# Optimization experiments

Measured on AMD Instinct MI355X. Metric: run time of the kernel, lower is better.

## Reference

```python
import jax, jax.numpy as jnp
import numpy as np

MARGIN = 0.2  # self.margin; temperature is unused in the original forward


def setup_inputs() -> dict:
    key = jax.random.key(0)
    k1, k2 = jax.random.split(key)
    B, D, NUM_CLASSES = 512, 256, 10
    features = jax.random.normal(k1, (B, D), dtype=jnp.float32)
    labels = jax.random.randint(k2, (B,), 0, NUM_CLASSES, dtype=jnp.int32)
    return {"features": features, "labels": labels}


def reference(features, labels):
    B = features.shape[0]
    sim = features @ features.T  # [B, B]

    eq = (labels[:, None] == labels[None, :])
    pos_mask = eq.astype(sim.dtype) * (1.0 - jnp.eye(B, dtype=sim.dtype))  # diag zeroed
    neg_mask = 1.0 - eq.astype(sim.dtype)

    # For anchor row i, pos j, neg k: relu(margin + sim[i,k] - sim[i,j])
    hinge = jax.nn.relu(MARGIN + sim[:, None, :] - sim[:, :, None])  # [B, Bpos, Bneg]
    loss_sum = jnp.einsum('ijk,ij,ik->', hinge, pos_mask, neg_mask)

    pos_cnt = pos_mask.sum(axis=1)  # per-row positive counts
    neg_cnt = neg_mask.sum(axis=1)
    valid = (pos_cnt > 0) & (neg_cnt > 0)
    num_valid = valid.sum().astype(sim.dtype)

    # Original bug faithfully reproduced: denominator uses the LAST row's
    # pos/neg counts (pos_sim/neg_sim leak out of the python loop).
    denom = num_valid * pos_cnt[-1] * neg_cnt[-1]
    return jnp.where(denom > 0, loss_sum / denom, jnp.zeros((), sim.dtype))
```

## Files before the change

kernel.cpp:

```cpp
#include <hip/hip_runtime.h>

#define B 512
#define D 256
#define NCLS 10
#define MARGIN 0.2f
#define THREADS 1024
#define NWAVES (THREADS / 64)
#define ROWS 2
#define NBLOCKS (B / ROWS)
#define DT 32
#define NDT (D / DT)
#define TILE_FLOATS (B * DT)

__global__ __launch_bounds__(THREADS) void fused_loss_kernel(
    const float* __restrict__ F, const int* __restrict__ labels,
    float* __restrict__ out)
{
    __shared__ float  buf[2][TILE_FLOATS];
    __shared__ float2 part[2][B];
    __shared__ float  pos_vals[ROWS][B + 4];
    __shared__ float  neg_vals[ROWS][B];
    __shared__ int    lbl[B];
    __shared__ int    cnt[ROWS][2];
    __shared__ int    hist[NCLS];
    __shared__ float  wred[NWAVES];
    __shared__ int    vred[NWAVES];

    const int t    = threadIdx.x;
    const int lane = t & 63;
    const int w    = t >> 6;
    const int i0   = blockIdx.x * ROWS;
    const int h    = t >> 9;
    const int j    = t & (B - 1);
    const int sj   = (j & 7) ^ ((j >> 3) & 7);
    const int h4   = __builtin_amdgcn_readfirstlane(h << 2);

    auto stage = [&](float* dstbase, int tile) {
#pragma unroll
        for (int k = 0; k < 4; ++k) {
            const int p  = (w << 8) + (k << 6) + lane;
            const int jj = p >> 3;
            const int e4 = (p & 7) ^ (jj & 7) ^ ((jj >> 3) & 7);
            const float* src = F + jj * D + tile * DT + (e4 << 2);
            float* dst = dstbase + (w << 10) + (k << 8);
            __builtin_amdgcn_global_load_lds(
                (const __attribute__((address_space(1))) void*)src,
                (__attribute__((address_space(3))) void*)dst, 16, 0, 0);
        }
    };

    if (t < B)        lbl[t] = labels[t];
    if (t < NCLS)     hist[t] = 0;
    if (t < ROWS * 2) ((int*)cnt)[t] = 0;
    stage(buf[0], 0);

    asm volatile("s_waitcnt lgkmcnt(0)" ::: "memory");
    __builtin_amdgcn_s_barrier();

    if (t < B) atomicAdd(&hist[lbl[t]], 1);

    float acc0 = 0.f, acc1 = 0.f;
    const float* Fa0 = F + (size_t)i0 * D;
    const float* Fa1 = Fa0 + D;
    int cur = 0;
    for (int tile = 0; tile < NDT; ++tile) {
        if (tile + 1 < NDT) {
            stage(buf[cur ^ 1], tile + 1);
            asm volatile("s_waitcnt vmcnt(4)" ::: "memory");
        } else {
            asm volatile("s_waitcnt vmcnt(0)" ::: "memory");
        }
        __builtin_amdgcn_s_barrier();
        __builtin_amdgcn_sched_barrier(0);
        const float* bufc = buf[cur];
        const int dt = tile * DT;
#pragma unroll
        for (int k = 0; k < 4; ++k) {
            const int e4 = h4 + k;
            const float4 x  = *(const float4*)&bufc[(j << 5) + ((e4 ^ sj) << 2)];
            const float4 a0 = *(const float4*)&Fa0[dt + (e4 << 2)];
            const float4 a1 = *(const float4*)&Fa1[dt + (e4 << 2)];
            acc0 = fmaf(a0.x, x.x, acc0); acc0 = fmaf(a0.y, x.y, acc0);
            acc0 = fmaf(a0.z, x.z, acc0); acc0 = fmaf(a0.w, x.w, acc0);
            acc1 = fmaf(a1.x, x.x, acc1); acc1 = fmaf(a1.y, x.y, acc1);
            acc1 = fmaf(a1.z, x.z, acc1); acc1 = fmaf(a1.w, x.w, acc1);
        }
        __builtin_amdgcn_sched_barrier(0);
        __builtin_amdgcn_s_barrier();
        cur ^= 1;
    }

    part[h][j] = make_float2(acc0, acc1);
    __syncthreads();
    const float2 pA = part[0][j];
    const float2 pB = part[1][j];
    const float  sv = h ? (pA.y + pB.y) : (pA.x + pB.x);

    {
        bool valid = false;
        if (t < B) { const int c = hist[lbl[t]]; valid = (c >= 2) && (c <= B - 1); }
        const unsigned long long mv = __ballot(valid);
        if (lane == 0) vred[w] = __popcll(mv);
    }

    const int r   = h;
    const int i_r = i0 + r;
    const int li  = lbl[i_r];
    {
        const bool active = (j != i_r);
        const bool ispos  = active && (lbl[j] == li);
        const bool isneg  = active && (lbl[j] != li);
        const unsigned long long mp = __ballot(ispos);
        const unsigned long long mn = __ballot(isneg);
        int basep = 0, basen = 0;
        if (lane == 0) {
            basep = atomicAdd(&cnt[r][0], __popcll(mp));
            basen = atomicAdd(&cnt[r][1], __popcll(mn));
        }
        basep = __shfl(basep, 0, 64);
        basen = __shfl(basen, 0, 64);
        const unsigned long long below = (1ull << lane) - 1ull;
        if (ispos) pos_vals[r][basep + __popcll(mp & below)] = sv;
        if (isneg) neg_vals[r][basen + __popcll(mn & below)] = sv;
    }
    __syncthreads();
    const int P = cnt[r][0], N = cnt[r][1];
    if (j < 4) pos_vals[r][P + j] = 1e30f;
    __syncthreads();

    const float nv_t = (j < N) ? neg_vals[r][j] : -1e30f;
    float local = 0.f;
    for (int pi = 0; pi < P; pi += 4) {
        const float4 pv = *(const float4*)&pos_vals[r][pi];
        float v;
        v = nv_t - (pv.x - MARGIN); local += (v > 0.f) ? v : 0.f;
        v = nv_t - (pv.y - MARGIN); local += (v > 0.f) ? v : 0.f;
        v = nv_t - (pv.z - MARGIN); local += (v > 0.f) ? v : 0.f;
        v = nv_t - (pv.w - MARGIN); local += (v > 0.f) ? v : 0.f;
    }

#pragma unroll
    for (int off = 32; off > 0; off >>= 1)
        local += __shfl_down(local, off, 64);
    if (lane == 0) wred[w] = local;
    __syncthreads();
    if (t == 0) {
        float s = 0.f;
        int   nv = 0;
#pragma unroll
        for (int k = 0; k < NWAVES; ++k) { s += wred[k]; nv += vred[k]; }
        const int   clast = hist[lbl[B - 1]];
        const float denom = (float)nv * (float)(clast - 1) * (float)(B - clast);
        atomicAdd(out, (denom > 0.f) ? s / denom : 0.f);
    }
}

extern "C" void kernel_launch(void* const* d_in, const int* in_sizes, int n_in,
                              void* d_out, int out_size, void* d_ws, size_t ws_size,
                              hipStream_t stream) {
    const float* F      = (const float*)d_in[0];
    const int*   labels = (const int*)d_in[1];
    float* out = (float*)d_out;
    (void)d_ws; (void)ws_size;

    fused_loss_kernel<<<NBLOCKS, THREADS, 0, stream>>>(F, labels, out);
}
```

Measured before the change: 73.89 us.

## Compute 2x2 register tile per thread with anchor rows cached in LDS

Remaps the Gram-row dot-product work so each thread computes two columns times two anchor rows over a quarter of each D tile, instead of one column over half. The two anchor rows are staged once into shared memory rather than re-read from global memory every tile. Partial sums are reduced across four slices through a buffer aliased onto the staging buffer. This is meant to raise arithmetic per LDS load and remove redundant global loads of the anchor rows. It adds a four-way reduction and reuses the staging buffer, which relies on the final barrier in the tile loop for correctness.

New measurement: 67.87 us (median of 2 runs). -8.1%, faster.

```diff
diff --git a/kernel.cpp b/kernel.cpp
--- a/kernel.cpp
+++ b/kernel.cpp
@@ -17,7 +17,7 @@
     float* __restrict__ out)
 {
     __shared__ float  buf[2][TILE_FLOATS];
-    __shared__ float2 part[2][B];
+    __shared__ float  fi[ROWS][D];
     __shared__ float  pos_vals[ROWS][B + 4];
     __shared__ float  neg_vals[ROWS][B];
     __shared__ int    lbl[B];
@@ -30,10 +30,12 @@
     const int lane = t & 63;
     const int w    = t >> 6;
     const int i0   = blockIdx.x * ROWS;
-    const int h    = t >> 9;
-    const int j    = t & (B - 1);
-    const int sj   = (j & 7) ^ ((j >> 3) & 7);
-    const int h4   = __builtin_amdgcn_readfirstlane(h << 2);
+    const int q    = t & 3;
+    const int g    = t >> 2;
+    const int j0   = 2 * g;
+    const int j1   = 2 * g + 1;
+    const int s0   = (j0 & 7) ^ ((j0 >> 3) & 7);
+    const int s1   = (j1 & 7) ^ ((j1 >> 3) & 7);
 
     auto stage = [&](float* dstbase, int tile) {
 #pragma unroll
@@ -52,6 +54,8 @@
     if (t < B)        lbl[t] = labels[t];
     if (t < NCLS)     hist[t] = 0;
     if (t < ROWS * 2) ((int*)cnt)[t] = 0;
+    if (t < (ROWS * D) / 4)
+        ((float4*)fi)[t] = ((const float4*)(F + (size_t)i0 * D))[t];
     stage(buf[0], 0);
 
     asm volatile("s_waitcnt lgkmcnt(0)" ::: "memory");
@@ -59,9 +63,7 @@
 
     if (t < B) atomicAdd(&hist[lbl[t]], 1);
 
-    float acc0 = 0.f, acc1 = 0.f;
-    const float* Fa0 = F + (size_t)i0 * D;
-    const float* Fa1 = Fa0 + D;
+    float acc00 = 0.f, acc01 = 0.f, acc10 = 0.f, acc11 = 0.f;
     int cur = 0;
     for (int tile = 0; tile < NDT; ++tile) {
         if (tile + 1 < NDT) {
@@ -75,26 +77,38 @@
         const float* bufc = buf[cur];
         const int dt = tile * DT;
 #pragma unroll
-        for (int k = 0; k < 4; ++k) {
-            const int e4 = h4 + k;
-            const float4 x  = *(const float4*)&bufc[(j << 5) + ((e4 ^ sj) << 2)];
-            const float4 a0 = *(const float4*)&Fa0[dt + (e4 << 2)];
-            const float4 a1 = *(const float4*)&Fa1[dt + (e4 << 2)];
-            acc0 = fmaf(a0.x, x.x, acc0); acc0 = fmaf(a0.y, x.y, acc0);
-            acc0 = fmaf(a0.z, x.z, acc0); acc0 = fmaf(a0.w, x.w, acc0);
-            acc1 = fmaf(a1.x, x.x, acc1); acc1 = fmaf(a1.y, x.y, acc1);
-            acc1 = fmaf(a1.z, x.z, acc1); acc1 = fmaf(a1.w, x.w, acc1);
+        for (int k = 0; k < 2; ++k) {
+            const int e4 = 2 * q + k;
+            const float4 x0 = *(const float4*)&bufc[(j0 << 5) + ((e4 ^ s0) << 2)];
+            const float4 x1 = *(const float4*)&bufc[(j1 << 5) + ((e4 ^ s1) << 2)];
+            const float4 a0 = *(const float4*)&fi[0][dt + (e4 << 2)];
+            const float4 a1 = *(const float4*)&fi[1][dt + (e4 << 2)];
+            acc00 = fmaf(a0.x, x0.x, acc00); acc00 = fmaf(a0.y, x0.y, acc00);
+            acc00 = fmaf(a0.z, x0.z, acc00); acc00 = fmaf(a0.w, x0.w, acc00);
+            acc01 = fmaf(a1.x, x0.x, acc01); acc01 = fmaf(a1.y, x0.y, acc01);
+            acc01 = fmaf(a1.z, x0.z, acc01); acc01 = fmaf(a1.w, x0.w, acc01);
+            acc10 = fmaf(a0.x, x1.x, acc10); acc10 = fmaf(a0.y, x1.y, acc10);
+            acc10 = fmaf(a0.z, x1.z, acc10); acc10 = fmaf(a0.w, x1.w, acc10);
+            acc11 = fmaf(a1.x, x1.x, acc11); acc11 = fmaf(a1.y, x1.y, acc11);
+            acc11 = fmaf(a1.z, x1.z, acc11); acc11 = fmaf(a1.w, x1.w, acc11);
         }
         __builtin_amdgcn_sched_barrier(0);
         __builtin_amdgcn_s_barrier();
         cur ^= 1;
     }
 
-    part[h][j] = make_float2(acc0, acc1);
+    float2* part = (float2*)buf[0];
+    part[(q << 9) + j0] = make_float2(acc00, acc01);
+    part[(q << 9) + j1] = make_float2(acc10, acc11);
     __syncthreads();
-    const float2 pA = part[0][j];
-    const float2 pB = part[1][j];
-    const float  sv = h ? (pA.y + pB.y) : (pA.x + pB.x);
+    const int j = t & (B - 1);
+    const int h = t >> 9;
+    const float2 p0 = part[(0 << 9) + j];
+    const float2 p1 = part[(1 << 9) + j];
+    const float2 p2 = part[(2 << 9) + j];
+    const float2 p3 = part[(3 << 9) + j];
+    const float sv = h ? (p0.y + p1.y + p2.y + p3.y)
+                       : (p0.x + p1.x + p2.x + p3.x);
 
     {
         bool valid = false;
```
